# Optimization experiments

Hardware: AMD Instinct MI355X
Metric: run time of the kernel (lower is better)

Reference implementation:

```python
import jax, jax.numpy as jnp
import numpy as np

V, E, H, B, T = 32000, 256, 256, 4, 512


def setup_inputs() -> dict:
    key = jax.random.key(0)
    ks = jax.random.split(key, 16)
    s = 0.02
    d = {
        "x": jax.random.randint(ks[0], (B, T), 0, V, dtype=jnp.int64 if jax.config.read('jax_enable_x64') else jnp.int32).astype(jnp.int32),
        "h": jnp.zeros((1, B, H), jnp.float32),
        "embed_W": jax.random.normal(ks[1], (V, E), jnp.float32) * s,
        "gru_w_ih": jax.random.normal(ks[2], (3 * H, E), jnp.float32) * s,
        "gru_b_ih": jnp.zeros((3 * H,), jnp.float32),
        "gru_w_hh": jax.random.normal(ks[3], (3 * H, H), jnp.float32) * s,
        "gru_b_hh": jnp.zeros((3 * H,), jnp.float32),
        "attn_w_W": jax.random.normal(ks[4], (H, H), jnp.float32) * s,
        "attn_w_b": jnp.zeros((H,), jnp.float32),
        "attn_u_W": jax.random.normal(ks[5], (H, H), jnp.float32) * s,
        "attn_u_b": jnp.zeros((H,), jnp.float32),
        "attn_v_W": jax.random.normal(ks[6], (1, H), jnp.float32) * s,
        "attn_v_b": jnp.zeros((1,), jnp.float32),
        "fc_W": jax.random.normal(ks[7], (V, 2 * H), jnp.float32) * s,
        "fc_b": jnp.zeros((V,), jnp.float32),
    }
    return d


def reference(x, h, embed_W, gru_w_ih, gru_b_ih, gru_w_hh, gru_b_hh,
              attn_w_W, attn_w_b, attn_u_W, attn_u_b, attn_v_W, attn_v_b,
              fc_W, fc_b):
    # Embedding (dropout is identity in eval mode)
    emb = embed_W[x]                                   # [B,T,E]
    # GRU (single layer, batch_first), PyTorch gate math
    xp = emb @ gru_w_ih.T + gru_b_ih                   # [B,T,3H]
    h0 = h[0]                                          # [B,H]

    def step(hc, xpt):
        hp = hc @ gru_w_hh.T + gru_b_hh
        xr, xz, xn = jnp.split(xpt, 3, axis=-1)
        hr, hz, hn = jnp.split(hp, 3, axis=-1)
        r = jax.nn.sigmoid(xr + hr)
        z = jax.nn.sigmoid(xz + hz)
        n = jnp.tanh(xn + r * hn)
        h_new = (1.0 - z) * n + z * hc
        return h_new, h_new

    h_last, outs = jax.lax.scan(step, h0, jnp.swapaxes(xp, 0, 1))
    out = jnp.swapaxes(outs, 0, 1)                     # [B,T,H]

    # Bahdanau additive attention with causal mask
    q = out @ attn_w_W.T + attn_w_b                    # [B,T,H]
    k = out @ attn_u_W.T + attn_u_b                    # [B,T,H]
    e = jnp.tanh(q[:, :, None, :] + k[:, None, :, :])  # [B,T,T,H] (big intermediate)
    scores = jnp.einsum('bijh,h->bij', e, attn_v_W[0]) + attn_v_b[0]
    Tq = scores.shape[-1]
    causal_mask = jnp.triu(jnp.ones((Tq, Tq), bool), k=1)
    scores = jnp.where(causal_mask, -jnp.inf, scores)
    attn = jax.nn.softmax(scores, axis=-1)             # [B,T,T]
    ctx = jnp.einsum('bij,bjh->bih', attn, out)        # [B,T,H]

    combined = jnp.concatenate([out, ctx], axis=-1)    # [B,T,2H]
    logits = combined @ fc_W.T + fc_b                  # [B,T,V]
    return logits, h_last[None]
```

## Files before the change

### kernel.cpp

```cpp
#include <hip/hip_runtime.h>
#include <cstdint>
#include <cstddef>

#define Vv 32000
#define Ee 256
#define Hh 256
#define Bb 4
#define Tt 512
#define Mm (Bb*Tt)

typedef unsigned int u32;
typedef unsigned short u16;
typedef unsigned long long u64;
typedef __bf16 bf16x8 __attribute__((ext_vector_type(8)));
typedef float f32x4 __attribute__((ext_vector_type(4)));

__device__ __forceinline__ u16 f2bf(float f) {
  u32 u = __float_as_uint(f);
  u32 r = (u + 0x7FFFu + ((u >> 16) & 1u)) >> 16;
  return (u16)r;
}

template<bool GATHER>
__global__ __launch_bounds__(256) void gemm_small(
    const float* __restrict__ A, const int* __restrict__ xidx,
    const float* __restrict__ W, const float* __restrict__ bias,
    float* __restrict__ C, int N)
{
  __shared__ float At[64][36];
  __shared__ float Wt[64][66];
  const int tid = threadIdx.x;
  const int m0 = blockIdx.x * 32;
  const int n0 = blockIdx.y * 64;
  const int tm = tid >> 5;
  const int tn = tid & 31;
  float acc[4][2] = {};

  for (int k0 = 0; k0 < 256; k0 += 64) {
    __syncthreads();
    #pragma unroll
    for (int r = 0; r < 2; ++r) {
      int idx = tid + r*256;
      int i  = idx >> 4;
      int c4 = idx & 15;
      const float* src;
      if (GATHER) src = A + (size_t)xidx[m0+i]*256 + k0 + c4*4;
      else        src = A + (size_t)(m0+i)*256 + k0 + c4*4;
      float4 v = *(const float4*)src;
      At[c4*4+0][i]=v.x; At[c4*4+1][i]=v.y; At[c4*4+2][i]=v.z; At[c4*4+3][i]=v.w;
    }
    #pragma unroll
    for (int r = 0; r < 4; ++r) {
      int idx = tid + r*256;
      int j  = idx >> 4;
      int c4 = idx & 15;
      float4 v = *(const float4*)(W + (size_t)(n0+j)*256 + k0 + c4*4);
      Wt[c4*4+0][j]=v.x; Wt[c4*4+1][j]=v.y; Wt[c4*4+2][j]=v.z; Wt[c4*4+3][j]=v.w;
    }
    __syncthreads();
    #pragma unroll 8
    for (int k = 0; k < 64; ++k) {
      float4 a = *(const float4*)&At[k][tm*4];
      float2 w = *(const float2*)&Wt[k][tn*2];
      acc[0][0] += a.x*w.x; acc[0][1] += a.x*w.y;
      acc[1][0] += a.y*w.x; acc[1][1] += a.y*w.y;
      acc[2][0] += a.z*w.x; acc[2][1] += a.z*w.y;
      acc[3][0] += a.w*w.x; acc[3][1] += a.w*w.y;
    }
  }
  #pragma unroll
  for (int i = 0; i < 4; ++i)
    #pragma unroll
    for (int j = 0; j < 2; ++j) {
      int m = m0 + tm*4 + i, n = n0 + tn*2 + j;
      C[(size_t)m*N + n] = acc[i][j] + bias[n];
    }
}

__global__ __launch_bounds__(192, 1) void gru_scan(
    const float* __restrict__ xp, const float* __restrict__ h0,
    const float* __restrict__ whh, const float* __restrict__ bhh,
    float* __restrict__ gout, u64* __restrict__ hpair)
{
  __shared__ __attribute__((aligned(16))) float hl[256];
  __shared__ float dl[96];

  const int tid = threadIdx.x;
  const int bid = blockIdx.x;
  const int b = bid >> 3;
  const int c = bid & 7;

  const int r = tid >> 1;
  const int q = tid & 1;
  const int grow = (r >> 5)*256 + c*32 + (r & 31);

  f32x4 w[32];
  {
    const f32x4* wp = (const f32x4*)(whh + (size_t)grow*256 + q*128);
    #pragma unroll
    for (int kk = 0; kk < 32; ++kk) w[kk] = wp[kk];
  }

  float b_r = 0.f, b_z = 0.f, b_n = 0.f;
  const int jg = c*32 + (tid & 31);
  if (tid < 32) { b_r = bhh[jg]; b_z = bhh[256+jg]; b_n = bhh[512+jg]; }

  for (int t = 0; t < Tt; ++t) {
    float xr = 0.f, xz = 0.f, xn = 0.f;
    if (tid < 32) {
      size_t xb = ((size_t)(b*Tt) + t)*768 + jg;
      xr = xp[xb]; xz = xp[xb+256]; xn = xp[xb+512];
    }

    if (tid < 64) {
      float4 hv;
      if (t == 0) {
        hv = *(const float4*)(h0 + b*Hh + tid*4);
      } else {
        const u64* src = hpair + ((size_t)(b*2) + ((t-1)&1))*256 + tid*4;
        const u32 want = (u32)t;
        u64 v0, v1, v2, v3;
        for (;;) {
          v0 = __hip_atomic_load(src+0, __ATOMIC_RELAXED, __HIP_MEMORY_SCOPE_AGENT);
          v1 = __hip_atomic_load(src+1, __ATOMIC_RELAXED, __HIP_MEMORY_SCOPE_AGENT);
          v2 = __hip_atomic_load(src+2, __ATOMIC_RELAXED, __HIP_MEMORY_SCOPE_AGENT);
          v3 = __hip_atomic_load(src+3, __ATOMIC_RELAXED, __HIP_MEMORY_SCOPE_AGENT);
          if ((u32)(v0 >> 32) == want && (u32)(v1 >> 32) == want &&
              (u32)(v2 >> 32) == want && (u32)(v3 >> 32) == want) break;
        }
        hv.x = __uint_as_float((u32)v0); hv.y = __uint_as_float((u32)v1);
        hv.z = __uint_as_float((u32)v2); hv.w = __uint_as_float((u32)v3);
      }
      *(float4*)&hl[tid*4] = hv;
    }
    __syncthreads();

    float s = 0.f;
    {
      const float* hp = &hl[q*128];
      #pragma unroll
      for (int kk = 0; kk < 32; ++kk) {
        float4 h4 = *(const float4*)(hp + kk*4);
        s += w[kk].x*h4.x + w[kk].y*h4.y + w[kk].z*h4.z + w[kk].w*h4.w;
      }
    }
    s += __shfl_xor(s, 1);
    if (q == 0) dl[r] = s;
    __syncthreads();

    if (tid < 32) {
      int j = tid;
      float dr = dl[j], dz = dl[32+j], dn = dl[64+j];
      float rr = 1.f/(1.f + __expf(-(xr + dr + b_r)));
      float zz = 1.f/(1.f + __expf(-(xz + dz + b_z)));
      float aa = xn + rr*(dn + b_n);
      float nn = 1.f - 2.f/(1.f + __expf(2.f*aa));
      float hp = hl[jg];
      float hn = (1.f - zz)*nn + zz*hp;
      u64 pv = ((u64)(u32)(t + 1) << 32) | (u64)__float_as_uint(hn);
      __hip_atomic_store(hpair + ((size_t)(b*2) + (t&1))*256 + jg, pv,
                         __ATOMIC_RELAXED, __HIP_MEMORY_SCOPE_AGENT);
      gout[((size_t)(b*Tt) + t)*Hh + jg] = hn;
    }
  }
}

__global__ __launch_bounds__(256) void attn_kernel(
    const float* __restrict__ outm, const float* __restrict__ qm,
    const float* __restrict__ km, const float* __restrict__ vW,
    const float* __restrict__ vb_p, float* __restrict__ ctx)
{
  __shared__ __attribute__((aligned(16))) float q[256];
  __shared__ __attribute__((aligned(16))) float vv[256];
  __shared__ float p[512];
  __shared__ float red[8];

  const int blk = blockIdx.x;
  const int b = blk >> 9;
  const int i = 511 - (blk & 511);
  const int tid = threadIdx.x;

  if (tid < 64) {
    ((float4*)q)[tid]  = ((const float4*)(qm + ((size_t)(b*Tt)+i)*Hh))[tid];
    ((float4*)vv)[tid] = ((const float4*)vW)[tid];
  }
  const float vb = vb_p[0];
  __syncthreads();

  for (int j = tid; j <= i; j += 256) {
    const float* kr = km + ((size_t)(b*Tt)+j)*Hh;
    float s = 0.f;
    #pragma unroll 4
    for (int h = 0; h < 256; h += 4) {
      float4 kv = *(const float4*)(kr + h);
      float x0 = q[h+0]+kv.x, x1 = q[h+1]+kv.y, x2 = q[h+2]+kv.z, x3 = q[h+3]+kv.w;
      s += vv[h+0]*(1.f - 2.f/(1.f + __expf(2.f*x0)));
      s += vv[h+1]*(1.f - 2.f/(1.f + __expf(2.f*x1)));
      s += vv[h+2]*(1.f - 2.f/(1.f + __expf(2.f*x2)));
      s += vv[h+3]*(1.f - 2.f/(1.f + __expf(2.f*x3)));
    }
    p[j] = s + vb;
  }
  __syncthreads();

  float m = -1e30f;
  for (int j = tid; j <= i; j += 256) m = fmaxf(m, p[j]);
  #pragma unroll
  for (int off = 32; off; off >>= 1) m = fmaxf(m, __shfl_xor(m, off));
  if ((tid & 63) == 0) red[tid >> 6] = m;
  __syncthreads();
  m = fmaxf(fmaxf(red[0], red[1]), fmaxf(red[2], red[3]));

  float s = 0.f;
  for (int j = tid; j <= i; j += 256) { float e = __expf(p[j]-m); p[j] = e; s += e; }
  #pragma unroll
  for (int off = 32; off; off >>= 1) s += __shfl_xor(s, off);
  if ((tid & 63) == 0) red[4 + (tid >> 6)] = s;
  __syncthreads();
  s = red[4]+red[5]+red[6]+red[7];
  const float inv = 1.f/s;

  float acc = 0.f;
  const float* op = outm + (size_t)(b*Tt)*Hh + tid;
  #pragma unroll 4
  for (int j = 0; j <= i; ++j) acc += p[j] * op[(size_t)j*Hh];
  ctx[((size_t)(b*Tt)+i)*Hh + tid] = acc*inv;
}

__global__ __launch_bounds__(256) void conv_w_bf16(
    const float* __restrict__ src, u16* __restrict__ dst, int n8)
{
  int i = blockIdx.x*256 + threadIdx.x;
  if (i < n8) {
    float4 a = ((const float4*)src)[i*2];
    float4 b = ((const float4*)src)[i*2+1];
    uint4 o;
    o.x = (u32)f2bf(a.x) | ((u32)f2bf(a.y) << 16);
    o.y = (u32)f2bf(a.z) | ((u32)f2bf(a.w) << 16);
    o.z = (u32)f2bf(b.x) | ((u32)f2bf(b.y) << 16);
    o.w = (u32)f2bf(b.z) | ((u32)f2bf(b.w) << 16);
    ((uint4*)dst)[i] = o;
  }
}

__global__ __launch_bounds__(256) void conv_comb_bf16(
    const float* __restrict__ gout, const float* __restrict__ ctx,
    u16* __restrict__ dst)
{
  int i = blockIdx.x*256 + threadIdx.x;
  int m  = i >> 6;
  int kg = (i & 63) * 8;
  const float* src = (kg < 256) ? (gout + (size_t)m*256 + kg)
                                : (ctx  + (size_t)m*256 + kg - 256);
  float4 a = *(const float4*)src;
  float4 b = *(const float4*)(src + 4);
  uint4 o;
  o.x = (u32)f2bf(a.x) | ((u32)f2bf(a.y) << 16);
  o.y = (u32)f2bf(a.z) | ((u32)f2bf(a.w) << 16);
  o.z = (u32)f2bf(b.x) | ((u32)f2bf(b.y) << 16);
  o.w = (u32)f2bf(b.z) | ((u32)f2bf(b.w) << 16);
  ((uint4*)dst)[i] = o;
}

__global__ __launch_bounds__(256) void fc_mfma(
    const u16* __restrict__ Ab, const u16* __restrict__ Wb,
    const float* __restrict__ bias, float* __restrict__ C)
{
  __shared__ __attribute__((aligned(16))) u16 As[128*32];
  __shared__ __attribute__((aligned(16))) u16 Bs[128*32];
  const int bid = blockIdx.x;
  const int mt = bid & 15, nt = bid >> 4;
  const int m0 = mt*128, n0 = nt*128;
  const int tid = threadIdx.x;
  const int wave = tid >> 6, lane = tid & 63;

  f32x4 acc[4][4];
  #pragma unroll
  for (int i = 0; i < 4; ++i)
    #pragma unroll
    for (int j = 0; j < 4; ++j)
      acc[i][j] = (f32x4){0.f, 0.f, 0.f, 0.f};

  const int wm = (wave & 1)*64;
  const int wn = (wave >> 1)*64;
  const int frow = lane & 15;
  const int fk   = (lane >> 4)*8;

  for (int k0 = 0; k0 < 512; k0 += 32) {
    __syncthreads();
    #pragma unroll
    for (int i = 0; i < 2; ++i) {
      int ebase = wave*1024 + i*512;
      int e = ebase + lane*8;
      int row = e >> 5, col = e & 31;
      __builtin_amdgcn_global_load_lds(
          (const __attribute__((address_space(1))) u32*)(Ab + (size_t)(m0+row)*512 + k0 + col),
          (__attribute__((address_space(3))) u32*)(As + ebase), 16, 0, 0);
      __builtin_amdgcn_global_load_lds(
          (const __attribute__((address_space(1))) u32*)(Wb + (size_t)(n0+row)*512 + k0 + col),
          (__attribute__((address_space(3))) u32*)(Bs + ebase), 16, 0, 0);
    }
    __syncthreads();

    bf16x8 af[4], bfr[4];
    #pragma unroll
    for (int mi = 0; mi < 4; ++mi)
      af[mi] = *(const bf16x8*)&As[(wm + mi*16 + frow)*32 + fk];
    #pragma unroll
    for (int ni = 0; ni < 4; ++ni)
      bfr[ni] = *(const bf16x8*)&Bs[(wn + ni*16 + frow)*32 + fk];
    #pragma unroll
    for (int mi = 0; mi < 4; ++mi)
      #pragma unroll
      for (int ni = 0; ni < 4; ++ni)
        acc[mi][ni] = __builtin_amdgcn_mfma_f32_16x16x32_bf16(af[mi], bfr[ni], acc[mi][ni], 0, 0, 0);
  }

  const int coln = lane & 15, rq = (lane >> 4)*4;
  #pragma unroll
  for (int ni = 0; ni < 4; ++ni) {
    int n = n0 + wn + ni*16 + coln;
    float bb = bias[n];
    #pragma unroll
    for (int mi = 0; mi < 4; ++mi) {
      int mbase = m0 + wm + mi*16 + rq;
      #pragma unroll
      for (int r2 = 0; r2 < 4; ++r2)
        C[(size_t)(mbase + r2)*Vv + n] = acc[mi][ni][r2] + bb;
    }
  }
}

__global__ void copy_hlast(const float* __restrict__ gout, float* __restrict__ dst)
{
  int idx = blockIdx.x*256 + threadIdx.x;
  if (idx < Bb*Hh) {
    int b = idx >> 8, h = idx & 255;
    dst[idx] = gout[((size_t)(b*Tt) + (Tt-1))*Hh + h];
  }
}

extern "C" void kernel_launch(void* const* d_in, const int* in_sizes, int n_in,
                              void* d_out, int out_size, void* d_ws, size_t ws_size,
                              hipStream_t stream)
{
  const int*   x    = (const int*)  d_in[0];
  const float* h0   = (const float*)d_in[1];
  const float* embW = (const float*)d_in[2];
  const float* wih  = (const float*)d_in[3];
  const float* bih  = (const float*)d_in[4];
  const float* whh  = (const float*)d_in[5];
  const float* bhh  = (const float*)d_in[6];
  const float* awW  = (const float*)d_in[7];
  const float* awb  = (const float*)d_in[8];
  const float* auW  = (const float*)d_in[9];
  const float* aub  = (const float*)d_in[10];
  const float* avW  = (const float*)d_in[11];
  const float* avb  = (const float*)d_in[12];
  const float* fcW  = (const float*)d_in[13];
  const float* fcb  = (const float*)d_in[14];
  float* outp = (float*)d_out;

  float* ws   = (float*)d_ws;
  float* xp   = ws;
  float* gout = xp   + (size_t)Mm*768;
  float* q    = gout + (size_t)Mm*Hh;
  float* k    = q    + (size_t)Mm*Hh;
  float* ctx  = k    + (size_t)Mm*Hh;
  u64*  hpair = (u64*)(ctx + (size_t)Mm*Hh);
  u16* comb = (u16*)(hpair + 2048);
  u16* Wb   = comb + (size_t)Mm*512;

  dim3 g1(Mm/32, 768/64);
  gemm_small<true><<<g1, 256, 0, stream>>>(embW, x, wih, bih, xp, 768);

  conv_w_bf16<<<8000, 256, 0, stream>>>(fcW, Wb, Vv*512/8);

  gru_scan<<<32, 192, 0, stream>>>(xp, h0, whh, bhh, gout, hpair);

  dim3 g3(Mm/32, 256/64);
  gemm_small<false><<<g3, 256, 0, stream>>>(gout, nullptr, awW, awb, q, 256);
  gemm_small<false><<<g3, 256, 0, stream>>>(gout, nullptr, auW, aub, k, 256);

  attn_kernel<<<Bb*Tt, 256, 0, stream>>>(gout, q, k, avW, avb, ctx);

  conv_comb_bf16<<<512, 256, 0, stream>>>(gout, ctx, comb);

  fc_mfma<<<16*250, 256, 0, stream>>>(comb, Wb, fcb, outp);

  copy_hlast<<<4, 256, 0, stream>>>(gout, outp + (size_t)Mm*Vv);
}
```

Measured before the change: 1.538 ms.

## Fold fc weight bf16 conversion into GRU scan launch on idle blocks

Removes the separate fc_W to bf16 conversion kernel and runs that conversion on 32 extra blocks of the GRU scan launch, so the memory-bound conversion overlaps the latency-bound sequential recurrence. The GRU recurrent weights are held as a scalar array pinned in registers with empty asm constraints. The dot product is split into four independent accumulators to shorten the serial FMA dependency chain per timestep. The risk is that the conversion blocks compete for memory bandwidth with the scan's cross-block spin-wait polling. The block index mapping is also changed.

```diff
diff --git a/kernel.cpp b/kernel.cpp
--- a/kernel.cpp
+++ b/kernel.cpp
@@ -80,26 +80,48 @@
 __global__ __launch_bounds__(192, 1) void gru_scan(
     const float* __restrict__ xp, const float* __restrict__ h0,
     const float* __restrict__ whh, const float* __restrict__ bhh,
-    float* __restrict__ gout, u64* __restrict__ hpair)
-{
+    float* __restrict__ gout, u64* __restrict__ hpair,
+    const float* __restrict__ fcW, u16* __restrict__ Wb)
+{
+  const int tid = threadIdx.x;
+  const int bid = blockIdx.x;
+  const int b = bid & 7;
+  const int c = bid >> 3;
+
+  if (b >= 4) {
+    const int cbid = (c << 2) | (b - 4);
+    const int n8 = Vv*512/8;
+    for (int i = cbid*192 + tid; i < n8; i += 32*192) {
+      float4 a = ((const float4*)fcW)[i*2];
+      float4 v = ((const float4*)fcW)[i*2+1];
+      uint4 o;
+      o.x = (u32)f2bf(a.x) | ((u32)f2bf(a.y) << 16);
+      o.y = (u32)f2bf(a.z) | ((u32)f2bf(a.w) << 16);
+      o.z = (u32)f2bf(v.x) | ((u32)f2bf(v.y) << 16);
+      o.w = (u32)f2bf(v.z) | ((u32)f2bf(v.w) << 16);
+      ((uint4*)Wb)[i] = o;
+    }
+    return;
+  }
+
   __shared__ __attribute__((aligned(16))) float hl[256];
   __shared__ float dl[96];
-
-  const int tid = threadIdx.x;
-  const int bid = blockIdx.x;
-  const int b = bid >> 3;
-  const int c = bid & 7;
 
   const int r = tid >> 1;
   const int q = tid & 1;
   const int grow = (r >> 5)*256 + c*32 + (r & 31);
 
-  f32x4 w[32];
+  float w[128];
   {
     const f32x4* wp = (const f32x4*)(whh + (size_t)grow*256 + q*128);
     #pragma unroll
-    for (int kk = 0; kk < 32; ++kk) w[kk] = wp[kk];
-  }
+    for (int kk = 0; kk < 32; ++kk) {
+      f32x4 v = wp[kk];
+      w[4*kk+0] = v.x; w[4*kk+1] = v.y; w[4*kk+2] = v.z; w[4*kk+3] = v.w;
+    }
+  }
+  #pragma unroll
+  for (int kk = 0; kk < 128; ++kk) asm volatile("" : "+v"(w[kk]));
 
   float b_r = 0.f, b_z = 0.f, b_n = 0.f;
   const int jg = c*32 + (tid & 31);
@@ -135,15 +157,19 @@
     }
     __syncthreads();
 
-    float s = 0.f;
+    float s0 = 0.f, s1 = 0.f, s2 = 0.f, s3 = 0.f;
     {
       const float* hp = &hl[q*128];
       #pragma unroll
       for (int kk = 0; kk < 32; ++kk) {
         float4 h4 = *(const float4*)(hp + kk*4);
-        s += w[kk].x*h4.x + w[kk].y*h4.y + w[kk].z*h4.z + w[kk].w*h4.w;
+        s0 += w[4*kk+0]*h4.x;
+        s1 += w[4*kk+1]*h4.y;
+        s2 += w[4*kk+2]*h4.z;
+        s3 += w[4*kk+3]*h4.w;
       }
     }
+    float s = (s0 + s1) + (s2 + s3);
     s += __shfl_xor(s, 1);
     if (q == 0) dl[r] = s;
     __syncthreads();
@@ -225,22 +251,6 @@
   #pragma unroll 4
   for (int j = 0; j <= i; ++j) acc += p[j] * op[(size_t)j*Hh];
   ctx[((size_t)(b*Tt)+i)*Hh + tid] = acc*inv;
-}
-
-__global__ __launch_bounds__(256) void conv_w_bf16(
-    const float* __restrict__ src, u16* __restrict__ dst, int n8)
-{
-  int i = blockIdx.x*256 + threadIdx.x;
-  if (i < n8) {
-    float4 a = ((const float4*)src)[i*2];
-    float4 b = ((const float4*)src)[i*2+1];
-    uint4 o;
-    o.x = (u32)f2bf(a.x) | ((u32)f2bf(a.y) << 16);
-    o.y = (u32)f2bf(a.z) | ((u32)f2bf(a.w) << 16);
-    o.z = (u32)f2bf(b.x) | ((u32)f2bf(b.y) << 16);
-    o.w = (u32)f2bf(b.z) | ((u32)f2bf(b.w) << 16);
-    ((uint4*)dst)[i] = o;
-  }
 }
 
 __global__ __launch_bounds__(256) void conv_comb_bf16(
@@ -374,9 +384,7 @@
   dim3 g1(Mm/32, 768/64);
   gemm_small<true><<<g1, 256, 0, stream>>>(embW, x, wih, bih, xp, 768);
 
-  conv_w_bf16<<<8000, 256, 0, stream>>>(fcW, Wb, Vv*512/8);
-
-  gru_scan<<<32, 192, 0, stream>>>(xp, h0, whh, bhh, gout, hpair);
+  gru_scan<<<64, 192, 0, stream>>>(xp, h0, whh, bhh, gout, hpair, fcW, Wb);
 
   dim3 g3(Mm/32, 256/64);
   gemm_small<false><<<g3, 256, 0, stream>>>(gout, nullptr, awW, awb, q, 256);
```

Measured after the change: 1.375 ms. -10.6%, faster.
